# Kernel tuning notes

Hardware: AMD Instinct MI355X
Metric: run time of the kernel (lower is better)

Reference implementation:

```python
import jax, jax.numpy as jnp
import numpy as np

DIM = 2048
NUM_HEADS = 16
NUM_KV_HEADS = 4
HEAD_DIM = DIM // NUM_HEADS  # 128
ROPE_BASE = 10000.0
CLIP = 31.0
BLOCK = 128


def fake_quant(w):
    """Blockwise int-ish fake quantization, steady QAT state (ratio=1, clip=31, no noise)."""
    out_f, in_f = w.shape
    pad = (-in_f) % BLOCK
    wp = jnp.pad(w, ((0, 0), (0, pad)))
    wb = wp.reshape(-1, BLOCK)
    # scale computed under no_grad in torch -> stop_gradient
    bmax = jnp.max(jnp.abs(wb), axis=1)
    s = jnp.maximum(bmax / CLIP, 1e-12).astype(jnp.float16)
    s = jnp.maximum(s, jnp.finfo(jnp.float16).tiny).astype(jnp.float32)
    s = jax.lax.stop_gradient(s)[:, None]
    ws = wb / s
    q = ws - jax.lax.stop_gradient(ws) + jax.lax.stop_gradient(
        jnp.round(jnp.clip(ws, -(CLIP + 1.0), CLIP)))  # STE
    qw = (q * s).reshape(out_f, in_f + pad)
    return qw[:, :in_f] if pad > 0 else qw


def rms_norm(x):
    eps = jnp.finfo(x.dtype).eps
    return x * jax.lax.rsqrt(jnp.mean(x * x, axis=-1, keepdims=True) + eps)


def rope_tables(seqlen, dtype):
    inv_freq = 1.0 / (ROPE_BASE ** (jnp.arange(0, HEAD_DIM, 2, dtype=jnp.float32) / HEAD_DIM))
    freqs = jnp.outer(jnp.arange(seqlen, dtype=jnp.float32), inv_freq)  # [S, hd/2]
    return jnp.cos(freqs).astype(dtype), jnp.sin(freqs).astype(dtype)


def apply_rotary(x, cos, sin):
    # x: [B,H,S,hd]; cos/sin: [S,hd/2]
    half = x.shape[-1] // 2
    x1, x2 = x[..., :half], x[..., half:]
    return jnp.concatenate((x1 * cos + x2 * sin, -x1 * sin + x2 * cos), axis=-1)


def setup_inputs() -> dict:
    key = jax.random.key(0)
    ks = jax.random.split(key, 6)
    kv_dim = NUM_KV_HEADS * HEAD_DIM
    std = DIM ** -0.5
    return {
        "x": jax.random.normal(ks[0], (2, 2048, DIM), dtype=jnp.float32),
        "Wq": jax.random.normal(ks[1], (DIM, DIM), dtype=jnp.float32) * std,
        "Wk": jax.random.normal(ks[2], (kv_dim, DIM), dtype=jnp.float32) * std,
        "Wv": jax.random.normal(ks[3], (kv_dim, DIM), dtype=jnp.float32) * std,
        "Wproj": jax.random.normal(ks[4], (DIM, DIM), dtype=jnp.float32) * std,
        "q_gain": jnp.full((NUM_HEADS,), 1.0, dtype=jnp.float32),
    }


def reference(x, Wq, Wk, Wv, Wproj, q_gain):
    B, S, D = x.shape
    H, KV, hd = NUM_HEADS, NUM_KV_HEADS, HEAD_DIM
    q = (x @ fake_quant(Wq).T).reshape(B, S, H, hd).transpose(0, 2, 1, 3)   # [B,H,S,hd]
    k = (x @ fake_quant(Wk).T).reshape(B, S, KV, hd).transpose(0, 2, 1, 3)  # [B,KV,S,hd]
    v = (x @ fake_quant(Wv).T).reshape(B, S, KV, hd).transpose(0, 2, 1, 3)
    q = rms_norm(q)
    k = rms_norm(k)
    cos, sin = rope_tables(S, q.dtype)
    q = apply_rotary(q, cos, sin)
    k = apply_rotary(k, cos, sin)
    q = q * q_gain[None, :, None, None]
    # GQA: expand kv heads
    rep = H // KV
    k = jnp.repeat(k, rep, axis=1)  # [B,H,S,hd]
    v = jnp.repeat(v, rep, axis=1)
    scale = 1.0 / jnp.sqrt(jnp.asarray(hd, dtype=q.dtype))
    scores = jnp.einsum("bhqd,bhkd->bhqk", q, k) * scale
    causal = jnp.tril(jnp.ones((S, S), dtype=bool))
    scores = jnp.where(causal, scores, jnp.asarray(-jnp.inf, dtype=scores.dtype))
    attn = jax.nn.softmax(scores, axis=-1)
    y = jnp.einsum("bhqk,bhkd->bhqd", attn, v)  # [B,H,S,hd]
    y = y.transpose(0, 2, 1, 3).reshape(B, S, D)
    return y @ fake_quant(Wproj).T
```

## Files before the change

kernel.cpp:

```cpp
#include <hip/hip_runtime.h>
#include <hip/hip_bf16.h>
#include <hip/hip_fp16.h>

#define SEQ    2048
#define DMODEL 2048
#define NH     16
#define NKV    4
#define HD     128
#define NTOT   3072
#define MROWS  4096

typedef __attribute__((ext_vector_type(4))) float f32x4;
typedef __attribute__((ext_vector_type(8))) __bf16 bf16x8;
typedef __attribute__((ext_vector_type(8))) unsigned short u16x8;
typedef __attribute__((ext_vector_type(4))) unsigned short u16x4;

__device__ __forceinline__ void async_copy16(const void* g, void* l) {
  __builtin_amdgcn_global_load_lds(
      (const __attribute__((address_space(1))) void*)g,
      (__attribute__((address_space(3))) void*)l, 16, 0, 0);
}

__device__ __forceinline__ unsigned short fto16(float f) {
  __hip_bfloat16 h = __float2bfloat16(f);
  return *(unsigned short*)&h;
}

__device__ __forceinline__ float b2f(unsigned short u) {
  unsigned int t = (unsigned int)u << 16;
  float f;
  __builtin_memcpy(&f, &t, 4);
  return f;
}

__global__ __launch_bounds__(256) void fq_kernel(const float* __restrict__ Wq,
                                                 const float* __restrict__ Wk,
                                                 const float* __restrict__ Wv,
                                                 const float* __restrict__ Wp,
                                                 unsigned short* __restrict__ Wcat,
                                                 unsigned short* __restrict__ Wpq) {
  int g = blockIdx.x * 4 + (threadIdx.x >> 6);
  int lane = threadIdx.x & 63;
  const float* W;
  unsigned short* out;
  int blk;
  if (g < 32768)      { W = Wq; out = Wcat;                          blk = g; }
  else if (g < 40960) { W = Wk; out = Wcat + (size_t)2048 * 2048;    blk = g - 32768; }
  else if (g < 49152) { W = Wv; out = Wcat + (size_t)2560 * 2048;    blk = g - 40960; }
  else                { W = Wp; out = Wpq;                           blk = g - 49152; }
  const float* p = W + (size_t)blk * 128 + lane * 2;
  float w0 = p[0], w1 = p[1];
  float m = fmaxf(fabsf(w0), fabsf(w1));
#pragma unroll
  for (int o = 32; o; o >>= 1) m = fmaxf(m, __shfl_xor(m, o));
  float s = fmaxf(m / 31.0f, 1e-12f);
  s = __half2float(__float2half(s));
  s = fmaxf(s, 6.103515625e-05f);
  float q0 = rintf(fminf(fmaxf(w0 / s, -32.0f), 31.0f)) * s;
  float q1 = rintf(fminf(fmaxf(w1 / s, -32.0f), 31.0f)) * s;
  unsigned short* o16 = out + (size_t)blk * 128 + lane * 2;
  o16[0] = fto16(q0);
  o16[1] = fto16(q1);
}

__global__ __launch_bounds__(256) void conv_kernel(const float* __restrict__ in,
                                                   unsigned short* __restrict__ out,
                                                   int n) {
  int i = (blockIdx.x * blockDim.x + threadIdx.x) * 4;
  if (i >= n) return;
  float4 v = *(const float4*)(in + i);
  ushort4 o;
  o.x = fto16(v.x); o.y = fto16(v.y); o.z = fto16(v.z); o.w = fto16(v.w);
  *(ushort4*)(out + i) = o;
}

#define BM 128
#define BN 128
#define BK 64
template <typename OT>
__global__ __launch_bounds__(256, 3) void gemm_bt(const unsigned short* __restrict__ A,
                                                  const unsigned short* __restrict__ Bm,
                                                  OT* __restrict__ C,
                                                  unsigned short* __restrict__ vtb,
                                                  int M, int N, int K) {
  __shared__ unsigned short As[BM * BK];
  __shared__ unsigned short Bs[BN * BK];
  const int tid = threadIdx.x;
  const int wave = tid >> 6, lane = tid & 63;
  const int quad = lane >> 4, l16 = lane & 15;

  int wg = blockIdx.y * gridDim.x + blockIdx.x;
  int nwg = gridDim.x * gridDim.y;
  int cpx = nwg >> 3;
  int swz = (wg & 7) * cpx + (wg >> 3);
  int bxs = swz % gridDim.x, bys = swz / gridDim.x;
  const int m0 = bxs * BM, n0 = bys * BN;
  const int wm = (wave >> 1) * 64, wn = (wave & 1) * 64;

  const unsigned short* Ag = A + (size_t)m0 * K;
  const unsigned short* Bg = Bm + (size_t)n0 * K;

  f32x4 acc[4][4];
#pragma unroll
  for (int i = 0; i < 4; i++)
#pragma unroll
    for (int j = 0; j < 4; j++) acc[i][j] = f32x4{0.f, 0.f, 0.f, 0.f};

  const int srow = tid >> 3;
  const int sg8 = (((lane & 7) ^ (lane >> 3))) * 8;
  const unsigned short* gA = Ag + (size_t)srow * K + sg8;
  const unsigned short* gB = Bg + (size_t)srow * K + sg8;
  unsigned short* lA = &As[wave * 512];
  unsigned short* lB = &Bs[wave * 512];

  for (int k0 = 0; k0 < K; k0 += BK) {
    __syncthreads();
#pragma unroll
    for (int c = 0; c < 4; ++c) async_copy16(gA + (size_t)c * 32 * K + k0, lA + c * 2048);
#pragma unroll
    for (int c = 0; c < 4; ++c) async_copy16(gB + (size_t)c * 32 * K + k0, lB + c * 2048);
    __syncthreads();
#pragma unroll
    for (int kk = 0; kk < 2; ++kk) {
      bf16x8 af[4], bf[4];
#pragma unroll
      for (int t = 0; t < 4; t++)
        af[t] = *(const bf16x8*)&As[(wm + t * 16 + l16) * BK + ((((kk << 2) + quad) ^ (l16 & 7)) << 3)];
#pragma unroll
      for (int t = 0; t < 4; t++)
        bf[t] = *(const bf16x8*)&Bs[(wn + t * 16 + l16) * BK + ((((kk << 2) + quad) ^ (l16 & 7)) << 3)];
#pragma unroll
      for (int i = 0; i < 4; i++)
#pragma unroll
        for (int j = 0; j < 4; j++)
          acc[i][j] = __builtin_amdgcn_mfma_f32_16x16x32_bf16(af[i], bf[j], acc[i][j], 0, 0, 0);
    }
  }

  const bool isv = (vtb != nullptr) && (n0 >= 2560);
  if (isv) {
    const int kvh = (n0 - 2560) >> 7;
#pragma unroll
    for (int i = 0; i < 4; i++) {
      int row0 = m0 + wm + i * 16 + quad * 4;
      int bz = row0 >> 11, s0 = row0 & 2047;
#pragma unroll
      for (int j = 0; j < 4; j++) {
        int d = wn + j * 16 + l16;
        u16x4 o;
#pragma unroll
        for (int r = 0; r < 4; r++) o[r] = fto16(acc[i][j][r]);
        *(u16x4*)&vtb[(size_t)((bz * NKV + kvh) * HD + d) * SEQ + s0] = o;
      }
    }
    return;
  }
#pragma unroll
  for (int i = 0; i < 4; i++) {
    int row_base = m0 + wm + i * 16 + quad * 4;
#pragma unroll
    for (int j = 0; j < 4; j++) {
      int col = n0 + wn + j * 16 + l16;
#pragma unroll
      for (int r = 0; r < 4; r++) {
        if constexpr (sizeof(OT) == 2)
          C[(size_t)(row_base + r) * N + col] = fto16(acc[i][j][r]);
        else
          C[(size_t)(row_base + r) * N + col] = acc[i][j][r];
      }
    }
  }
}

#define QSCALE 0.12751791437524245f
#define NEG_L2RB_64 (-0.2076205059304601f)
__global__ __launch_bounds__(256) void normrope_kernel(const unsigned short* __restrict__ qkvb,
                                                       const float* __restrict__ qgain,
                                                       unsigned short* __restrict__ qbuf,
                                                       unsigned short* __restrict__ kbuf) {
  const int i = blockIdx.x;
  const int bz = i >> 11, tok = i & 2047;
  const int wave = threadIdx.x >> 6, lane = threadIdx.x & 63;
  const unsigned short* row = qkvb + (size_t)i * NTOT;

  float invf = exp2f((float)lane * NEG_L2RB_64);
  float freq = (float)tok * invf;
  float cs = cosf(freq), sn = sinf(freq);

  for (int slot = wave; slot < 20; slot += 4) {
    if (slot < 16) {
      int hh = slot;
      const unsigned short* src = row + hh * HD;
      float x1 = b2f(src[lane]), x2 = b2f(src[lane + 64]);
      float ss = x1 * x1 + x2 * x2;
#pragma unroll
      for (int o = 32; o; o >>= 1) ss += __shfl_xor(ss, o);
      float rn = rsqrtf(ss * (1.0f / 128.0f) + 1.1920929e-07f);
      float n1 = x1 * rn, n2 = x2 * rn;
      float g = qgain[hh] * QSCALE;
      unsigned short* dst = qbuf + ((size_t)(bz * NH + hh) * SEQ + tok) * HD;
      dst[lane]      = fto16((n1 * cs + n2 * sn) * g);
      dst[lane + 64] = fto16((-n1 * sn + n2 * cs) * g);
    } else {
      int hh = slot - 16;
      const unsigned short* src = row + DMODEL + hh * HD;
      float x1 = b2f(src[lane]), x2 = b2f(src[lane + 64]);
      float ss = x1 * x1 + x2 * x2;
#pragma unroll
      for (int o = 32; o; o >>= 1) ss += __shfl_xor(ss, o);
      float rn = rsqrtf(ss * (1.0f / 128.0f) + 1.1920929e-07f);
      float n1 = x1 * rn, n2 = x2 * rn;
      unsigned short* dst = kbuf + ((size_t)(bz * NKV + hh) * SEQ + tok) * HD;
      dst[lane]      = fto16(n1 * cs + n2 * sn);
      dst[lane + 64] = fto16(-n1 * sn + n2 * cs);
    }
  }
}

__global__ __launch_bounds__(512, 4) void attn_kernel(const unsigned short* __restrict__ qb,
                                                      const unsigned short* __restrict__ kb,
                                                      const unsigned short* __restrict__ vtb,
                                                      unsigned short* __restrict__ yb) {
  __shared__ unsigned short Ks[2][64 * 128];
  __shared__ unsigned short Vt[128 * 64];
  __shared__ unsigned short Ps[8][16 * 64];

  const int bx = blockIdx.x;
  const int h = blockIdx.y;
  const int bz = blockIdx.z;
  const int qt = bz ? bx : (15 - bx);
  const int tid = threadIdx.x;
  const int wave = tid >> 6, lane = tid & 63;
  const int quad = lane >> 4, l16 = lane & 15;
  const int q0 = qt * 128;
  const int base = q0 + wave * 16;
  const int kdiag = base >> 6;

  const unsigned short* qg = qb + (size_t)(bz * NH + h) * SEQ * HD;
  const unsigned short* kg = kb + (size_t)(bz * NKV + (h >> 2)) * SEQ * HD;
  const unsigned short* vg = vtb + (size_t)(bz * NKV + (h >> 2)) * HD * SEQ;
  unsigned short* psw = &Ps[wave][0];

  bf16x8 qf[4];
#pragma unroll
  for (int ds = 0; ds < 4; ++ds)
    qf[ds] = *(const bf16x8*)(qg + (size_t)(base + l16) * HD + ds * 32 + quad * 8);

  f32x4 oacc[8];
#pragma unroll
  for (int j = 0; j < 8; ++j) oacc[j] = f32x4{0.f, 0.f, 0.f, 0.f};
  float m_i = -__builtin_inff();
  float l_i = 0.f;

  const int krow0 = wave * 4 + (lane >> 4);
  const int ksrcg = (lane & 15) ^ (krow0 & 15);
  const unsigned short* kgK = kg + (size_t)krow0 * HD + ksrcg * 8;

  const int vdw = tid >> 3, vgr = tid & 7;

  const int nkt = 2 * qt + 2;

  async_copy16(kgK, &Ks[0][wave * 512]);
  async_copy16(kgK + (size_t)32 * HD, &Ks[0][4096 + wave * 512]);
  u16x8 pv[2];
#pragma unroll
  for (int i = 0; i < 2; ++i)
    pv[i] = *(const u16x8*)(vg + (size_t)(i * 64 + vdw) * SEQ + vgr * 8);

  for (int kt = 0; kt < nkt; ++kt) {
    __syncthreads();
#pragma unroll
    for (int i = 0; i < 2; ++i) {
      int d = i * 64 + vdw;
      *(u16x8*)&Vt[d * 64 + ((vgr ^ (d & 7)) << 3)] = pv[i];
    }
    if (kt + 1 < nkt) {
      const unsigned short* s = kgK + (size_t)(kt + 1) * 64 * HD;
      async_copy16(s, &Ks[(kt + 1) & 1][wave * 512]);
      async_copy16(s + (size_t)32 * HD, &Ks[(kt + 1) & 1][4096 + wave * 512]);
    }
    __asm__ volatile("s_waitcnt lgkmcnt(0)" ::: "memory");
    __builtin_amdgcn_sched_barrier(0);
    __asm__ volatile("s_barrier" ::: "memory");

    if (kt + 1 < nkt) {
#pragma unroll
      for (int i = 0; i < 2; ++i)
        pv[i] = *(const u16x8*)(vg + (size_t)(i * 64 + vdw) * SEQ + (kt + 1) * 64 + vgr * 8);
    }

    if (kt <= kdiag) {
      const unsigned short* Kc = Ks[kt & 1];
      f32x4 st[4];
#pragma unroll
      for (int mt = 0; mt < 4; ++mt) st[mt] = f32x4{0.f, 0.f, 0.f, 0.f};
      __builtin_amdgcn_s_setprio(1);
#pragma unroll
      for (int mt = 0; mt < 4; ++mt)
#pragma unroll
        for (int ds = 0; ds < 4; ++ds) {
          bf16x8 kf = *(const bf16x8*)&Kc[(mt * 16 + l16) * 128 + ((((ds << 2) + quad) ^ l16) << 3)];
          st[mt] = __builtin_amdgcn_mfma_f32_16x16x32_bf16(kf, qf[ds], st[mt], 0, 0, 0);
        }
      __builtin_amdgcn_s_setprio(0);

      const int qrow = base + l16;
      float p[4][4];
      float mx = -__builtin_inff();
      if (kt == kdiag) {
#pragma unroll
        for (int mt = 0; mt < 4; ++mt)
#pragma unroll
          for (int r = 0; r < 4; ++r) {
            int kp = kt * 64 + mt * 16 + quad * 4 + r;
            float v = (kp <= qrow) ? st[mt][r] : -__builtin_inff();
            p[mt][r] = v;
            mx = fmaxf(mx, v);
          }
      } else {
#pragma unroll
        for (int mt = 0; mt < 4; ++mt)
#pragma unroll
          for (int r = 0; r < 4; ++r) {
            p[mt][r] = st[mt][r];
            mx = fmaxf(mx, st[mt][r]);
          }
      }
      mx = fmaxf(mx, __shfl_xor(mx, 16));
      mx = fmaxf(mx, __shfl_xor(mx, 32));
      float mnew = (mx > m_i + 8.f) ? mx : m_i;
      float rs = 0.f;
#pragma unroll
      for (int mt = 0; mt < 4; ++mt)
#pragma unroll
        for (int r = 0; r < 4; ++r) {
          float e = exp2f(p[mt][r] - mnew);
          p[mt][r] = e;
          rs += e;
        }
      rs += __shfl_xor(rs, 16);
      rs += __shfl_xor(rs, 32);
      if (mnew != m_i) {
        float a = exp2f(m_i - mnew);
#pragma unroll
        for (int j = 0; j < 8; ++j) oacc[j] *= a;
        l_i = l_i * a + rs;
        m_i = mnew;
      } else {
        l_i += rs;
      }

#pragma unroll
      for (int mt = 0; mt < 4; ++mt) {
        u16x4 w;
#pragma unroll
        for (int r = 0; r < 4; ++r) w[r] = fto16(p[mt][r]);
        int g = mt * 2 + (quad >> 1);
        *(u16x4*)&psw[l16 * 64 + ((g ^ (l16 & 7)) << 3) + (quad & 1) * 4] = w;
      }

      __asm__ volatile("s_waitcnt lgkmcnt(0)" ::: "memory");

      __builtin_amdgcn_s_setprio(1);
#pragma unroll
      for (int c = 0; c < 2; ++c) {
        bf16x8 pf = *(const bf16x8*)&psw[l16 * 64 + ((((c << 2) + quad) ^ (l16 & 7)) << 3)];
#pragma unroll
        for (int mt = 0; mt < 8; ++mt) {
          bf16x8 vf = *(const bf16x8*)&Vt[(mt * 16 + l16) * 64 + ((((c << 2) + quad) ^ (l16 & 7)) << 3)];
          oacc[mt] = __builtin_amdgcn_mfma_f32_16x16x32_bf16(vf, pf, oacc[mt], 0, 0, 0);
        }
      }
      __builtin_amdgcn_s_setprio(0);
    }
  }

  {
    float il = 1.0f / l_i;
    int qrow = base + l16;
#pragma unroll
    for (int mt = 0; mt < 8; ++mt) {
      u16x4 o;
#pragma unroll
      for (int r = 0; r < 4; ++r) o[r] = fto16(oacc[mt][r] * il);
      *(u16x4*)&yb[(size_t)(bz * SEQ + qrow) * DMODEL + h * HD + mt * 16 + quad * 4] = o;
    }
  }
}

extern "C" void kernel_launch(void* const* d_in, const int* in_sizes, int n_in,
                              void* d_out, int out_size, void* d_ws, size_t ws_size,
                              hipStream_t stream) {
  (void)in_sizes; (void)n_in; (void)out_size; (void)ws_size;
  const float* x  = (const float*)d_in[0];
  const float* Wq = (const float*)d_in[1];
  const float* Wk = (const float*)d_in[2];
  const float* Wv = (const float*)d_in[3];
  const float* Wp = (const float*)d_in[4];
  const float* qg = (const float*)d_in[5];
  float* out = (float*)d_out;
  char* ws = (char*)d_ws;

  unsigned short* xb   = (unsigned short*)(ws + 0);
  unsigned short* Wcat = (unsigned short*)(ws + 16777216);
  unsigned short* Wpq  = (unsigned short*)(ws + 29360128);
  unsigned short* qkvb = (unsigned short*)(ws + 37748736);
  unsigned short* qbuf = (unsigned short*)(ws + 62914560);
  unsigned short* kbuf = (unsigned short*)(ws + 79691776);
  unsigned short* vtb  = (unsigned short*)(ws + 83886080);
  unsigned short* yb   = xb;

  fq_kernel<<<81920 / 4, 256, 0, stream>>>(Wq, Wk, Wv, Wp, Wcat, Wpq);
  conv_kernel<<<8388608 / 1024, 256, 0, stream>>>(x, xb, 8388608);
  gemm_bt<unsigned short><<<dim3(32, 24), 256, 0, stream>>>(xb, Wcat, qkvb, vtb, MROWS, NTOT, DMODEL);
  normrope_kernel<<<MROWS, 256, 0, stream>>>(qkvb, qg, qbuf, kbuf);
  attn_kernel<<<dim3(16, NH, 2), 512, 0, stream>>>(qbuf, kbuf, vtb, yb);
  gemm_bt<float><<<dim3(32, 16), 256, 0, stream>>>(yb, Wpq, out, nullptr, MROWS, DMODEL, DMODEL);
}
```

Baseline: 302.3 us.

## Fuse RMSNorm+RoPE into QKV GEMM epilogue and merge prep kernels

The QKV GEMM epilogue now stages each 128x128 bf16 tile in LDS transposed, then applies per-head RMSNorm, RoPE and q_gain in place and writes q/k directly. This removes the intermediate qkv buffer round trip and the separate normrope launch. Weight fake-quant, x conversion and cos/sin table generation are merged into one prep kernel, saving launches. In exchange the GEMM uses a bit more LDS and carries a longer serialized epilogue that reads the cos/sin tables from global memory.

```diff
diff --git a/kernel.cpp b/kernel.cpp
--- a/kernel.cpp
+++ b/kernel.cpp
@@ -33,58 +33,80 @@
   return f;
 }
 
-__global__ __launch_bounds__(256) void fq_kernel(const float* __restrict__ Wq,
-                                                 const float* __restrict__ Wk,
-                                                 const float* __restrict__ Wv,
-                                                 const float* __restrict__ Wp,
-                                                 unsigned short* __restrict__ Wcat,
-                                                 unsigned short* __restrict__ Wpq) {
-  int g = blockIdx.x * 4 + (threadIdx.x >> 6);
-  int lane = threadIdx.x & 63;
-  const float* W;
-  unsigned short* out;
-  int blk;
-  if (g < 32768)      { W = Wq; out = Wcat;                          blk = g; }
-  else if (g < 40960) { W = Wk; out = Wcat + (size_t)2048 * 2048;    blk = g - 32768; }
-  else if (g < 49152) { W = Wv; out = Wcat + (size_t)2560 * 2048;    blk = g - 40960; }
-  else                { W = Wp; out = Wpq;                           blk = g - 49152; }
-  const float* p = W + (size_t)blk * 128 + lane * 2;
-  float w0 = p[0], w1 = p[1];
-  float m = fmaxf(fabsf(w0), fabsf(w1));
-#pragma unroll
-  for (int o = 32; o; o >>= 1) m = fmaxf(m, __shfl_xor(m, o));
-  float s = fmaxf(m / 31.0f, 1e-12f);
-  s = __half2float(__float2half(s));
-  s = fmaxf(s, 6.103515625e-05f);
-  float q0 = rintf(fminf(fmaxf(w0 / s, -32.0f), 31.0f)) * s;
-  float q1 = rintf(fminf(fmaxf(w1 / s, -32.0f), 31.0f)) * s;
-  unsigned short* o16 = out + (size_t)blk * 128 + lane * 2;
-  o16[0] = fto16(q0);
-  o16[1] = fto16(q1);
-}
-
-__global__ __launch_bounds__(256) void conv_kernel(const float* __restrict__ in,
-                                                   unsigned short* __restrict__ out,
-                                                   int n) {
-  int i = (blockIdx.x * blockDim.x + threadIdx.x) * 4;
-  if (i >= n) return;
-  float4 v = *(const float4*)(in + i);
-  ushort4 o;
-  o.x = fto16(v.x); o.y = fto16(v.y); o.z = fto16(v.z); o.w = fto16(v.w);
-  *(ushort4*)(out + i) = o;
+#define QSCALE 0.12751791437524245f
+#define NEG_L2RB_64 (-0.2076205059304601f)
+
+#define NFQ   20480
+#define NCONV 8192
+#define NROPE 512
+__global__ __launch_bounds__(256) void prep_kernel(const float* __restrict__ Wq,
+                                                   const float* __restrict__ Wk,
+                                                   const float* __restrict__ Wv,
+                                                   const float* __restrict__ Wp,
+                                                   const float* __restrict__ x,
+                                                   unsigned short* __restrict__ Wcat,
+                                                   unsigned short* __restrict__ Wpq,
+                                                   unsigned short* __restrict__ xb,
+                                                   float* __restrict__ CS,
+                                                   float* __restrict__ SN) {
+  const int bid = blockIdx.x;
+  const int tid = threadIdx.x;
+  if (bid < NFQ) {
+    int g = bid * 4 + (tid >> 6);
+    int lane = tid & 63;
+    const float* W;
+    unsigned short* out;
+    int blk;
+    if (g < 32768)      { W = Wq; out = Wcat;                          blk = g; }
+    else if (g < 40960) { W = Wk; out = Wcat + (size_t)2048 * 2048;    blk = g - 32768; }
+    else if (g < 49152) { W = Wv; out = Wcat + (size_t)2560 * 2048;    blk = g - 40960; }
+    else                { W = Wp; out = Wpq;                           blk = g - 49152; }
+    const float* p = W + (size_t)blk * 128 + lane * 2;
+    float w0 = p[0], w1 = p[1];
+    float m = fmaxf(fabsf(w0), fabsf(w1));
+#pragma unroll
+    for (int o = 32; o; o >>= 1) m = fmaxf(m, __shfl_xor(m, o));
+    float s = fmaxf(m / 31.0f, 1e-12f);
+    s = __half2float(__float2half(s));
+    s = fmaxf(s, 6.103515625e-05f);
+    float q0 = rintf(fminf(fmaxf(w0 / s, -32.0f), 31.0f)) * s;
+    float q1 = rintf(fminf(fmaxf(w1 / s, -32.0f), 31.0f)) * s;
+    unsigned short* o16 = out + (size_t)blk * 128 + lane * 2;
+    o16[0] = fto16(q0);
+    o16[1] = fto16(q1);
+  } else if (bid < NFQ + NCONV) {
+    int i = ((bid - NFQ) * 256 + tid) * 4;
+    float4 v = *(const float4*)(x + i);
+    ushort4 o;
+    o.x = fto16(v.x); o.y = fto16(v.y); o.z = fto16(v.z); o.w = fto16(v.w);
+    *(ushort4*)(xb + i) = o;
+  } else {
+    int idx = (bid - NFQ - NCONV) * 256 + tid;
+    int t = idx >> 6, l = idx & 63;
+    float invf = exp2f((float)l * NEG_L2RB_64);
+    float fr = (float)t * invf;
+    CS[idx] = cosf(fr);
+    SN[idx] = sinf(fr);
+  }
 }
 
 #define BM 128
 #define BN 128
 #define BK 64
-template <typename OT>
+template <typename OT, bool FUSED>
 __global__ __launch_bounds__(256, 3) void gemm_bt(const unsigned short* __restrict__ A,
                                                   const unsigned short* __restrict__ Bm,
                                                   OT* __restrict__ C,
                                                   unsigned short* __restrict__ vtb,
+                                                  unsigned short* __restrict__ qbuf,
+                                                  unsigned short* __restrict__ kbuf,
+                                                  const float* __restrict__ qgain,
+                                                  const float* __restrict__ CS,
+                                                  const float* __restrict__ SN,
                                                   int M, int N, int K) {
-  __shared__ unsigned short As[BM * BK];
-  __shared__ unsigned short Bs[BN * BK];
+  __shared__ unsigned short SH[FUSED ? 16896 : 16384];
+  unsigned short* As = SH;
+  unsigned short* Bs = SH + 8192;
   const int tid = threadIdx.x;
   const int wave = tid >> 6, lane = tid & 63;
   const int quad = lane >> 4, l16 = lane & 15;
@@ -137,24 +159,73 @@
     }
   }
 
-  const bool isv = (vtb != nullptr) && (n0 >= 2560);
-  if (isv) {
-    const int kvh = (n0 - 2560) >> 7;
+  if constexpr (FUSED) {
+    if (n0 >= 2560) {
+      const int kvh = (n0 - 2560) >> 7;
+#pragma unroll
+      for (int i = 0; i < 4; i++) {
+        int row0 = m0 + wm + i * 16 + quad * 4;
+        int bz = row0 >> 11, s0 = row0 & 2047;
+#pragma unroll
+        for (int j = 0; j < 4; j++) {
+          int d = wn + j * 16 + l16;
+          u16x4 o;
+#pragma unroll
+          for (int r = 0; r < 4; r++) o[r] = fto16(acc[i][j][r]);
+          *(u16x4*)&vtb[(size_t)((bz * NKV + kvh) * HD + d) * SEQ + s0] = o;
+        }
+      }
+      return;
+    }
+    __syncthreads();
 #pragma unroll
     for (int i = 0; i < 4; i++) {
-      int row0 = m0 + wm + i * 16 + quad * 4;
-      int bz = row0 >> 11, s0 = row0 & 2047;
+      int tok0 = wm + i * 16 + quad * 4;
 #pragma unroll
       for (int j = 0; j < 4; j++) {
         int d = wn + j * 16 + l16;
-        u16x4 o;
-#pragma unroll
-        for (int r = 0; r < 4; r++) o[r] = fto16(acc[i][j][r]);
-        *(u16x4*)&vtb[(size_t)((bz * NKV + kvh) * HD + d) * SEQ + s0] = o;
+        u16x4 w;
+#pragma unroll
+        for (int r = 0; r < 4; r++) w[r] = fto16(acc[i][j][r]);
+        *(u16x4*)&SH[d * 132 + tok0] = w;
+      }
+    }
+    __syncthreads();
+    const bool isq = (n0 < 2048);
+    const int hh = isq ? (n0 >> 7) : ((n0 - 2048) >> 7);
+    const float g = isq ? qgain[hh] * QSCALE : 1.0f;
+#pragma unroll 1
+    for (int gr = 0; gr < 8; ++gr) {
+      int tk = wave * 32 + gr * 4;
+      u16x4 a = *(const u16x4*)&SH[lane * 132 + tk];
+      u16x4 b = *(const u16x4*)&SH[(lane + 64) * 132 + tk];
+      float x1[4], x2[4], ss[4];
+#pragma unroll
+      for (int r = 0; r < 4; r++) {
+        x1[r] = b2f(a[r]); x2[r] = b2f(b[r]);
+        ss[r] = x1[r] * x1[r] + x2[r] * x2[r];
+      }
+#pragma unroll
+      for (int o = 32; o; o >>= 1)
+#pragma unroll
+        for (int r = 0; r < 4; r++) ss[r] += __shfl_xor(ss[r], o);
+#pragma unroll
+      for (int r = 0; r < 4; r++) {
+        int gt = m0 + tk + r;
+        int bz = gt >> 11, tokg = gt & 2047;
+        float rn = rsqrtf(ss[r] * (1.0f / 128.0f) + 1.1920929e-07f);
+        float cs = CS[tokg * 64 + lane], sn = SN[tokg * 64 + lane];
+        float n1 = x1[r] * rn, n2 = x2[r] * rn;
+        unsigned short* dst = isq
+            ? qbuf + ((size_t)(bz * NH + hh) * SEQ + tokg) * HD
+            : kbuf + ((size_t)(bz * NKV + hh) * SEQ + tokg) * HD;
+        dst[lane]      = fto16((n1 * cs + n2 * sn) * g);
+        dst[lane + 64] = fto16((-n1 * sn + n2 * cs) * g);
       }
     }
     return;
   }
+
 #pragma unroll
   for (int i = 0; i < 4; i++) {
     int row_base = m0 + wm + i * 16 + quad * 4;
@@ -168,51 +239,6 @@
         else
           C[(size_t)(row_base + r) * N + col] = acc[i][j][r];
       }
-    }
-  }
-}
-
-#define QSCALE 0.12751791437524245f
-#define NEG_L2RB_64 (-0.2076205059304601f)
-__global__ __launch_bounds__(256) void normrope_kernel(const unsigned short* __restrict__ qkvb,
-                                                       const float* __restrict__ qgain,
-                                                       unsigned short* __restrict__ qbuf,
-                                                       unsigned short* __restrict__ kbuf) {
-  const int i = blockIdx.x;
-  const int bz = i >> 11, tok = i & 2047;
-  const int wave = threadIdx.x >> 6, lane = threadIdx.x & 63;
-  const unsigned short* row = qkvb + (size_t)i * NTOT;
-
-  float invf = exp2f((float)lane * NEG_L2RB_64);
-  float freq = (float)tok * invf;
-  float cs = cosf(freq), sn = sinf(freq);
-
-  for (int slot = wave; slot < 20; slot += 4) {
-    if (slot < 16) {
-      int hh = slot;
-      const unsigned short* src = row + hh * HD;
-      float x1 = b2f(src[lane]), x2 = b2f(src[lane + 64]);
-      float ss = x1 * x1 + x2 * x2;
-#pragma unroll
-      for (int o = 32; o; o >>= 1) ss += __shfl_xor(ss, o);
-      float rn = rsqrtf(ss * (1.0f / 128.0f) + 1.1920929e-07f);
-      float n1 = x1 * rn, n2 = x2 * rn;
-      float g = qgain[hh] * QSCALE;
-      unsigned short* dst = qbuf + ((size_t)(bz * NH + hh) * SEQ + tok) * HD;
-      dst[lane]      = fto16((n1 * cs + n2 * sn) * g);
-      dst[lane + 64] = fto16((-n1 * sn + n2 * cs) * g);
-    } else {
-      int hh = slot - 16;
-      const unsigned short* src = row + DMODEL + hh * HD;
-      float x1 = b2f(src[lane]), x2 = b2f(src[lane + 64]);
-      float ss = x1 * x1 + x2 * x2;
-#pragma unroll
-      for (int o = 32; o; o >>= 1) ss += __shfl_xor(ss, o);
-      float rn = rsqrtf(ss * (1.0f / 128.0f) + 1.1920929e-07f);
-      float n1 = x1 * rn, n2 = x2 * rn;
-      unsigned short* dst = kbuf + ((size_t)(bz * NKV + hh) * SEQ + tok) * HD;
-      dst[lane]      = fto16(n1 * cs + n2 * sn);
-      dst[lane + 64] = fto16(-n1 * sn + n2 * cs);
     }
   }
 }
@@ -404,16 +430,20 @@
   unsigned short* xb   = (unsigned short*)(ws + 0);
   unsigned short* Wcat = (unsigned short*)(ws + 16777216);
   unsigned short* Wpq  = (unsigned short*)(ws + 29360128);
-  unsigned short* qkvb = (unsigned short*)(ws + 37748736);
+  float*          CS   = (float*)(ws + 37748736);
+  float*          SN   = (float*)(ws + 38273024);
   unsigned short* qbuf = (unsigned short*)(ws + 62914560);
   unsigned short* kbuf = (unsigned short*)(ws + 79691776);
   unsigned short* vtb  = (unsigned short*)(ws + 83886080);
   unsigned short* yb   = xb;
 
-  fq_kernel<<<81920 / 4, 256, 0, stream>>>(Wq, Wk, Wv, Wp, Wcat, Wpq);
-  conv_kernel<<<8388608 / 1024, 256, 0, stream>>>(x, xb, 8388608);
-  gemm_bt<unsigned short><<<dim3(32, 24), 256, 0, stream>>>(xb, Wcat, qkvb, vtb, MROWS, NTOT, DMODEL);
-  normrope_kernel<<<MROWS, 256, 0, stream>>>(qkvb, qg, qbuf, kbuf);
+  prep_kernel<<<NFQ + NCONV + NROPE, 256, 0, stream>>>(Wq, Wk, Wv, Wp, x,
+                                                       Wcat, Wpq, xb, CS, SN);
+  gemm_bt<unsigned short, true><<<dim3(32, 24), 256, 0, stream>>>(
+      xb, Wcat, (unsigned short*)nullptr, vtb, qbuf, kbuf, qg, CS, SN,
+      MROWS, NTOT, DMODEL);
   attn_kernel<<<dim3(16, NH, 2), 512, 0, stream>>>(qbuf, kbuf, vtb, yb);
-  gemm_bt<float><<<dim3(32, 16), 256, 0, stream>>>(yb, Wpq, out, nullptr, MROWS, DMODEL, DMODEL);
-}
+  gemm_bt<float, false><<<dim3(32, 16), 256, 0, stream>>>(
+      yb, Wpq, out, nullptr, nullptr, nullptr, nullptr, nullptr, nullptr,
+      MROWS, DMODEL, DMODEL);
+}
```

Result: faster. 292.2 us (-3.3%).
